# Kernel optimization log

Hardware: AMD Instinct MI355X
Metric: run time of the kernel (lower is better)

Reference implementation:

```python
import jax, jax.numpy as jnp
import numpy as np

H = 10          # hidden_size
TAIL = 1440     # slice out[:, -1440:-1, :]


def _cell(x, h, c, w_ih, w_hh, b):
    # PyTorch LSTM gate order: i, f, g, o
    gates = x @ w_ih.T + h @ w_hh.T + b          # [B, 4H]
    i, f, g, o = jnp.split(gates, 4, axis=-1)
    c = jax.nn.sigmoid(f) * c + jax.nn.sigmoid(i) * jnp.tanh(g)
    h = jax.nn.sigmoid(o) * jnp.tanh(c)
    return h, c


def setup_inputs() -> dict:
    key = jax.random.key(0)
    ks = jax.random.split(key, 13)
    s = 1.0 / np.sqrt(H)  # PyTorch default init range

    def u(k, shape):
        return jax.random.uniform(k, shape, jnp.float32, -s, s)

    return {
        "x": jax.random.normal(ks[0], (4096, 2048), jnp.float32),
        "w_ih0": u(ks[1], (4 * H, 1)),
        "w_hh0": u(ks[2], (4 * H, H)),
        "b_ih0": u(ks[3], (4 * H,)),
        "b_hh0": u(ks[4], (4 * H,)),
        "w_ih1": u(ks[5], (4 * H, H)),
        "w_hh1": u(ks[6], (4 * H, H)),
        "b_ih1": u(ks[7], (4 * H,)),
        "b_hh1": u(ks[8], (4 * H,)),
        "fc1_w": u(ks[9], (6, H)),
        "fc1_b": u(ks[10], (6,)),
        "fc2_w": u(ks[11], (1, 6)),
        "fc2_b": u(ks[12], (1,)),
    }


def reference(x, w_ih0, w_hh0, b_ih0, b_hh0, w_ih1, w_hh1, b_ih1, b_hh1,
              fc1_w, fc1_b, fc2_w, fc2_b):
    B, T = x.shape
    xt = x[..., None].transpose(1, 0, 2)         # [T, B, 1] time-major
    b0 = b_ih0 + b_hh0
    b1 = b_ih1 + b_hh1
    z = jnp.zeros((B, H), x.dtype)

    def step(carry, xi):
        h0, c0, h1, c1 = carry
        h0, c0 = _cell(xi, h0, c0, w_ih0, w_hh0, b0)
        h1, c1 = _cell(h0, h1, c1, w_ih1, w_hh1, b1)
        return (h0, c0, h1, c1), h1

    _, ys = jax.lax.scan(step, (z, z, z, z), xt)  # ys: [T, B, H]
    out = ys.transpose(1, 0, 2)[:, T - TAIL:T - 1, :]   # [B, 1439, H]
    out = jnp.tanh(out @ fc1_w.T + fc1_b)                # [B, 1439, 6]
    out = out @ fc2_w.T + fc2_b                          # [B, 1439, 1]
    return out[..., 0]                                   # [B, 1439]
```

## Files before the change

kernel.cpp:

```cpp
#include <hip/hip_runtime.h>

typedef float v2f __attribute__((ext_vector_type(2)));

#define T_LEN 2048
#define NH    10
#define OUT_T 1439
#define TFIRST 608
#define NSEQ  4096
#define CH    8
#define NCH   (T_LEN / CH)
#define MFIRST (TFIRST / CH)

static __device__ __forceinline__ v2f fma2(v2f a, v2f b, v2f c) {
  return __builtin_elementwise_fma(a, b, c);
}
static __device__ __forceinline__ v2f splat2(float v) { v2f r; r.x = v; r.y = v; return r; }
static __device__ __forceinline__ v2f mulsp(v2f a, float s) { v2f r; r.x = a.x*s; r.y = a.y*s; return r; }

static __device__ __forceinline__ float fast_sigmoid(float z) {
  float e = __builtin_amdgcn_exp2f(z * -1.4426950408889634f);
  return __builtin_amdgcn_rcpf(1.0f + e);
}
static __device__ __forceinline__ float fast_tanh(float z) {
  float e = __builtin_amdgcn_exp2f(z * -2.8853900817779268f);
  return __builtin_amdgcn_rcpf(1.0f + e) * 2.0f - 1.0f;
}

#define ROR_F(v, N) __uint_as_float(__builtin_amdgcn_update_dpp( \
    0, (int)__float_as_uint(v), 0x120 + (N), 0xF, 0xF, true))

__global__ void __launch_bounds__(192, 3)
lstm_fused(const float* __restrict__ x,
           const float* __restrict__ w_ih0, const float* __restrict__ w_hh0,
           const float* __restrict__ b_ih0, const float* __restrict__ b_hh0,
           const float* __restrict__ w_ih1, const float* __restrict__ w_hh1,
           const float* __restrict__ b_ih1, const float* __restrict__ b_hh1,
           const float* __restrict__ fc1_w, const float* __restrict__ fc1_b,
           const float* __restrict__ fc2_w, const float* __restrict__ fc2_b,
           float* __restrict__ out)
{
  __shared__ __align__(16) float h0buf[2][CH][64];
  __shared__ __align__(16) float h1buf[2][CH][64];

  const int tid  = threadIdx.x;
  const int wid  = tid / 64;
  const int lane = tid & 63;
  const int grp  = lane >> 4;
  const int u    = lane & 15;
  const int seq  = (int)blockIdx.x * 4 + grp;

  v2f wIF[NH], wGO[NH], vIF[NH], vGO[NH];
  v2f wx_if, wx_go, bb_if, bb_go;
  wx_if = wx_go = bb_if = bb_go = splat2(0.f);
#pragma unroll
  for (int j = 0; j < NH; ++j) {
    wIF[j] = splat2(0.f); wGO[j] = splat2(0.f);
    vIF[j] = splat2(0.f); vGO[j] = splat2(0.f);
  }
  float fcw[NH];
#pragma unroll
  for (int j = 0; j < NH; ++j) fcw[j] = 0.f;
  float fcb = 0.f, fc2wl = 0.f;
  const float fc2bl = fc2_b[0];

  if (wid == 0) {
    if (u < NH) {
      const int ri = 0*NH+u, rf = 1*NH+u, rg = 2*NH+u, ro = 3*NH+u;
      wx_if.x = w_ih0[ri]; wx_if.y = w_ih0[rf];
      wx_go.x = w_ih0[rg]; wx_go.y = w_ih0[ro];
      bb_if.x = b_ih0[ri] + b_hh0[ri]; bb_if.y = b_ih0[rf] + b_hh0[rf];
      bb_go.x = b_ih0[rg] + b_hh0[rg]; bb_go.y = b_ih0[ro] + b_hh0[ro];
#pragma unroll
      for (int j = 0; j < NH; ++j) {
        wIF[j].x = w_hh0[ri*NH+j]; wIF[j].y = w_hh0[rf*NH+j];
        wGO[j].x = w_hh0[rg*NH+j]; wGO[j].y = w_hh0[ro*NH+j];
      }
    }
  } else if (wid == 1) {
    if (u < NH) {
      const int ri = 0*NH+u, rf = 1*NH+u, rg = 2*NH+u, ro = 3*NH+u;
      bb_if.x = b_ih1[ri] + b_hh1[ri]; bb_if.y = b_ih1[rf] + b_hh1[rf];
      bb_go.x = b_ih1[rg] + b_hh1[rg]; bb_go.y = b_ih1[ro] + b_hh1[ro];
#pragma unroll
      for (int j = 0; j < NH; ++j) {
        wIF[j].x = w_ih1[ri*NH+j]; wIF[j].y = w_ih1[rf*NH+j];
        wGO[j].x = w_ih1[rg*NH+j]; wGO[j].y = w_ih1[ro*NH+j];
        vIF[j].x = w_hh1[ri*NH+j]; vIF[j].y = w_hh1[rf*NH+j];
        vGO[j].x = w_hh1[rg*NH+j]; vGO[j].y = w_hh1[ro*NH+j];
      }
    }
  } else {
    if (u < 6) {
      fcb = fc1_b[u]; fc2wl = fc2_w[u];
#pragma unroll
      for (int j = 0; j < NH; ++j) fcw[j] = fc1_w[u*NH + j];
    }
  }

  const float* xp   = x + (size_t)seq * T_LEN;
  float*       outp = out + (size_t)seq * OUT_T;

  float c = 0.f;
  float r0=0.f,r1=0.f,r2=0.f,r3=0.f,r4=0.f,r5=0.f,r6=0.f,r7=0.f,r8=0.f,r9=0.f;

  auto a_chunk = [&](int m) {
    float* hb = &h0buf[m & 1][0][0];
    const float* hr = &h0buf[m & 1][0][grp * 16];
    const float* xq = xp + m * CH;
#pragma unroll
    for (int s = 0; s < CH; ++s) {
      const float xv = xq[s];
      v2f aA = fma2(wx_if, splat2(xv), bb_if);
      v2f gA = fma2(wx_go, splat2(xv), bb_go);
      v2f aB = mulsp(wIF[1], r1);
      v2f gB = mulsp(wGO[1], r1);
#define L0T(j, hv, AC, GC) { const v2f sp = splat2(hv); \
      AC = fma2(wIF[j], sp, AC); GC = fma2(wGO[j], sp, GC); }
      L0T(0,r0,aA,gA) L0T(2,r2,aA,gA) L0T(3,r3,aB,gB) L0T(4,r4,aA,gA)
      L0T(5,r5,aB,gB) L0T(6,r6,aA,gA) L0T(7,r7,aB,gB) L0T(8,r8,aA,gA)
      L0T(9,r9,aB,gB)
#undef L0T
      const v2f gif = aA + aB;
      const v2f ggo = gA + gB;
      const float si = fast_sigmoid(gif.x);
      const float sf = fast_sigmoid(gif.y);
      const float tg = fast_tanh(ggo.x);
      const float so = fast_sigmoid(ggo.y);
      c = sf * c + si * tg;
      const float h0n = so * fast_tanh(c);
      hb[s*64 + lane] = h0n;
      const float4 va = *(const float4*)(hr + s*64);
      const float4 vb = *(const float4*)(hr + s*64 + 4);
      const float2 vc = *(const float2*)(hr + s*64 + 8);
      r0=va.x; r1=va.y; r2=va.z; r3=va.w;
      r4=vb.x; r5=vb.y; r6=vb.z; r7=vb.w;
      r8=vc.x; r9=vc.y;
    }
  };

  auto b_chunk = [&](int m) {
    const float* hbi = &h0buf[m & 1][0][grp * 16];
    float* ob = &h1buf[m & 1][0][0];
    const float* orr = &h1buf[m & 1][0][grp * 16];
#pragma unroll
    for (int s = 0; s < CH; ++s) {
      const float4 pa = *(const float4*)(hbi + s*64);
      const float4 pb = *(const float4*)(hbi + s*64 + 4);
      const float2 pc = *(const float2*)(hbi + s*64 + 8);
      v2f cA = fma2(wIF[0], splat2(pa.x), bb_if);
      v2f hA = fma2(wGO[0], splat2(pa.x), bb_go);
      v2f cB = mulsp(wIF[1], pa.y);
      v2f hB = mulsp(wGO[1], pa.y);
#define L1I(j, hv, AC, GC) { const v2f sp = splat2(hv); \
      AC = fma2(wIF[j], sp, AC); GC = fma2(wGO[j], sp, GC); }
      L1I(2,pa.z,cA,hA) L1I(3,pa.w,cB,hB) L1I(4,pb.x,cA,hA) L1I(5,pb.y,cB,hB)
      L1I(6,pb.z,cA,hA) L1I(7,pb.w,cB,hB) L1I(8,pc.x,cA,hA) L1I(9,pc.y,cB,hB)
#undef L1I
      v2f cC = mulsp(vIF[0], r0);
      v2f hC = mulsp(vGO[0], r0);
      v2f cD = mulsp(vIF[1], r1);
      v2f hD = mulsp(vGO[1], r1);
#define L1R(j, hv, AC, GC) { const v2f sp = splat2(hv); \
      AC = fma2(vIF[j], sp, AC); GC = fma2(vGO[j], sp, GC); }
      L1R(2,r2,cC,hC) L1R(3,r3,cD,hD) L1R(4,r4,cC,hC) L1R(5,r5,cD,hD)
      L1R(6,r6,cC,hC) L1R(7,r7,cD,hD) L1R(8,r8,cC,hC) L1R(9,r9,cD,hD)
#undef L1R
      const v2f gif = (cA + cB) + (cC + cD);
      const v2f ggo = (hA + hB) + (hC + hD);
      const float si1 = fast_sigmoid(gif.x);
      const float sf1 = fast_sigmoid(gif.y);
      const float tg1 = fast_tanh(ggo.x);
      const float so1 = fast_sigmoid(ggo.y);
      c = sf1 * c + si1 * tg1;
      const float h1n = so1 * fast_tanh(c);
      ob[s*64 + lane] = h1n;
      const float4 va = *(const float4*)(orr + s*64);
      const float4 vb = *(const float4*)(orr + s*64 + 4);
      const float2 vc = *(const float2*)(orr + s*64 + 8);
      r0=va.x; r1=va.y; r2=va.z; r3=va.w;
      r4=vb.x; r5=vb.y; r6=vb.z; r7=vb.w;
      r8=vc.x; r9=vc.y;
    }
  };

  auto c_chunk = [&](int m) {
    const float* hb = &h1buf[m & 1][0][grp * 16];
    const int t0 = m * CH;
    float* oq = outp + (t0 - TFIRST);
#pragma unroll
    for (int s = 0; s < CH; ++s) {
      if (t0 + s < TFIRST + OUT_T) {
        const float4 pa = *(const float4*)(hb + s*64);
        const float4 pb = *(const float4*)(hb + s*64 + 4);
        const float2 pc = *(const float2*)(hb + s*64 + 8);
        float acc = __builtin_fmaf(pa.x, fcw[0], fcb);
        acc = __builtin_fmaf(pa.y, fcw[1], acc);
        acc = __builtin_fmaf(pa.z, fcw[2], acc);
        acc = __builtin_fmaf(pa.w, fcw[3], acc);
        acc = __builtin_fmaf(pb.x, fcw[4], acc);
        acc = __builtin_fmaf(pb.y, fcw[5], acc);
        acc = __builtin_fmaf(pb.z, fcw[6], acc);
        acc = __builtin_fmaf(pb.w, fcw[7], acc);
        acc = __builtin_fmaf(pc.x, fcw[8], acc);
        acc = __builtin_fmaf(pc.y, fcw[9], acc);
        float y = fast_tanh(acc) * fc2wl;
        y += ROR_F(y, 8);
        y += ROR_F(y, 4);
        y += ROR_F(y, 2);
        y += ROR_F(y, 1);
        if (u == 0) oq[s] = y + fc2bl;
      }
    }
  };

#pragma unroll 1
  for (int r = 0; r < NCH + 2; ++r) {
    if (wid == 0) {
      if (r < NCH) a_chunk(r);
    } else if (wid == 1) {
      if (r >= 1 && r < NCH + 1) b_chunk(r - 1);
    } else {
      const int m = r - 2;
      if (m >= MFIRST && m < NCH) c_chunk(m);
    }
    __syncthreads();
  }
}

extern "C" void kernel_launch(void* const* d_in, const int* in_sizes, int n_in,
                              void* d_out, int out_size, void* d_ws, size_t ws_size,
                              hipStream_t stream) {
  const float* x     = (const float*)d_in[0];
  const float* w_ih0 = (const float*)d_in[1];
  const float* w_hh0 = (const float*)d_in[2];
  const float* b_ih0 = (const float*)d_in[3];
  const float* b_hh0 = (const float*)d_in[4];
  const float* w_ih1 = (const float*)d_in[5];
  const float* w_hh1 = (const float*)d_in[6];
  const float* b_ih1 = (const float*)d_in[7];
  const float* b_hh1 = (const float*)d_in[8];
  const float* fc1_w = (const float*)d_in[9];
  const float* fc1_b = (const float*)d_in[10];
  const float* fc2_w = (const float*)d_in[11];
  const float* fc2_b = (const float*)d_in[12];
  float* out = (float*)d_out;

  lstm_fused<<<dim3(NSEQ / 4), dim3(192), 0, stream>>>(
      x, w_ih0, w_hh0, b_ih0, b_hh0, w_ih1, w_hh1, b_ih1, b_hh1,
      fc1_w, fc1_b, fc2_w, fc2_b, out);
}
```

Measured before the change: 735.7 us.

## Fold activation scales into weights, merge FC into layer-0 wave, double chunk size

Pre-scales the LSTM and FC weights and biases by the exp2 constants for sigmoid and tanh. This removes a multiply per activation and lets the cell state be kept pre-scaled, so tanh(c) needs no extra scale. The FC head work moves from a dedicated third wave into the layer-0 wave, shrinking the block to 128 threads. The chunk size doubles to halve the number of block barriers, and x is loaded as float4 vectors. In exchange, the layer-0 wave now does both the recurrence and the FC head each round, which may lengthen its critical path.

```diff
diff --git a/kernel.cpp b/kernel.cpp
--- a/kernel.cpp
+++ b/kernel.cpp
@@ -7,29 +7,26 @@
 #define OUT_T 1439
 #define TFIRST 608
 #define NSEQ  4096
-#define CH    8
+#define CH    16
 #define NCH   (T_LEN / CH)
 #define MFIRST (TFIRST / CH)
 
+#define KSIG (-1.4426950408889634f)
+#define KTAN (-2.8853900817779268f)
+
 static __device__ __forceinline__ v2f fma2(v2f a, v2f b, v2f c) {
   return __builtin_elementwise_fma(a, b, c);
 }
 static __device__ __forceinline__ v2f splat2(float v) { v2f r; r.x = v; r.y = v; return r; }
 static __device__ __forceinline__ v2f mulsp(v2f a, float s) { v2f r; r.x = a.x*s; r.y = a.y*s; return r; }
-
-static __device__ __forceinline__ float fast_sigmoid(float z) {
-  float e = __builtin_amdgcn_exp2f(z * -1.4426950408889634f);
+static __device__ __forceinline__ float rcp1p(float e) {
   return __builtin_amdgcn_rcpf(1.0f + e);
-}
-static __device__ __forceinline__ float fast_tanh(float z) {
-  float e = __builtin_amdgcn_exp2f(z * -2.8853900817779268f);
-  return __builtin_amdgcn_rcpf(1.0f + e) * 2.0f - 1.0f;
 }
 
 #define ROR_F(v, N) __uint_as_float(__builtin_amdgcn_update_dpp( \
     0, (int)__float_as_uint(v), 0x120 + (N), 0xF, 0xF, true))
 
-__global__ void __launch_bounds__(192, 3)
+__global__ void __launch_bounds__(128, 2)
 lstm_fused(const float* __restrict__ x,
            const float* __restrict__ w_ih0, const float* __restrict__ w_hh0,
            const float* __restrict__ b_ih0, const float* __restrict__ b_hh0,
@@ -43,7 +40,7 @@
   __shared__ __align__(16) float h1buf[2][CH][64];
 
   const int tid  = threadIdx.x;
-  const int wid  = tid / 64;
+  const int wid  = tid >> 6;
   const int lane = tid & 63;
   const int grp  = lane >> 4;
   const int u    = lane & 15;
@@ -60,40 +57,41 @@
   float fcw[NH];
 #pragma unroll
   for (int j = 0; j < NH; ++j) fcw[j] = 0.f;
-  float fcb = 0.f, fc2wl = 0.f;
+  float fcb = 0.f, fc2w2 = 0.f, fc2wn = 0.f;
   const float fc2bl = fc2_b[0];
 
   if (wid == 0) {
     if (u < NH) {
       const int ri = 0*NH+u, rf = 1*NH+u, rg = 2*NH+u, ro = 3*NH+u;
-      wx_if.x = w_ih0[ri]; wx_if.y = w_ih0[rf];
-      wx_go.x = w_ih0[rg]; wx_go.y = w_ih0[ro];
-      bb_if.x = b_ih0[ri] + b_hh0[ri]; bb_if.y = b_ih0[rf] + b_hh0[rf];
-      bb_go.x = b_ih0[rg] + b_hh0[rg]; bb_go.y = b_ih0[ro] + b_hh0[ro];
+      wx_if.x = KSIG * w_ih0[ri];            wx_if.y = KSIG * w_ih0[rf];
+      wx_go.x = KTAN * w_ih0[rg];            wx_go.y = KSIG * w_ih0[ro];
+      bb_if.x = KSIG * (b_ih0[ri] + b_hh0[ri]); bb_if.y = KSIG * (b_ih0[rf] + b_hh0[rf]);
+      bb_go.x = KTAN * (b_ih0[rg] + b_hh0[rg]); bb_go.y = KSIG * (b_ih0[ro] + b_hh0[ro]);
 #pragma unroll
       for (int j = 0; j < NH; ++j) {
-        wIF[j].x = w_hh0[ri*NH+j]; wIF[j].y = w_hh0[rf*NH+j];
-        wGO[j].x = w_hh0[rg*NH+j]; wGO[j].y = w_hh0[ro*NH+j];
+        wIF[j].x = KSIG * w_hh0[ri*NH+j]; wIF[j].y = KSIG * w_hh0[rf*NH+j];
+        wGO[j].x = KTAN * w_hh0[rg*NH+j]; wGO[j].y = KSIG * w_hh0[ro*NH+j];
       }
     }
-  } else if (wid == 1) {
+    if (u < 6) {
+      fcb = KTAN * fc1_b[u];
+      const float w2 = fc2_w[u];
+      fc2w2 = 2.f * w2; fc2wn = -w2;
+#pragma unroll
+      for (int j = 0; j < NH; ++j) fcw[j] = KTAN * fc1_w[u*NH + j];
+    }
+  } else {
     if (u < NH) {
       const int ri = 0*NH+u, rf = 1*NH+u, rg = 2*NH+u, ro = 3*NH+u;
-      bb_if.x = b_ih1[ri] + b_hh1[ri]; bb_if.y = b_ih1[rf] + b_hh1[rf];
-      bb_go.x = b_ih1[rg] + b_hh1[rg]; bb_go.y = b_ih1[ro] + b_hh1[ro];
+      bb_if.x = KSIG * (b_ih1[ri] + b_hh1[ri]); bb_if.y = KSIG * (b_ih1[rf] + b_hh1[rf]);
+      bb_go.x = KTAN * (b_ih1[rg] + b_hh1[rg]); bb_go.y = KSIG * (b_ih1[ro] + b_hh1[ro]);
 #pragma unroll
       for (int j = 0; j < NH; ++j) {
-        wIF[j].x = w_ih1[ri*NH+j]; wIF[j].y = w_ih1[rf*NH+j];
-        wGO[j].x = w_ih1[rg*NH+j]; wGO[j].y = w_ih1[ro*NH+j];
-        vIF[j].x = w_hh1[ri*NH+j]; vIF[j].y = w_hh1[rf*NH+j];
-        vGO[j].x = w_hh1[rg*NH+j]; vGO[j].y = w_hh1[ro*NH+j];
+        wIF[j].x = KSIG * w_ih1[ri*NH+j]; wIF[j].y = KSIG * w_ih1[rf*NH+j];
+        wGO[j].x = KTAN * w_ih1[rg*NH+j]; wGO[j].y = KSIG * w_ih1[ro*NH+j];
+        vIF[j].x = KSIG * w_hh1[ri*NH+j]; vIF[j].y = KSIG * w_hh1[rf*NH+j];
+        vGO[j].x = KTAN * w_hh1[rg*NH+j]; vGO[j].y = KSIG * w_hh1[ro*NH+j];
       }
-    }
-  } else {
-    if (u < 6) {
-      fcb = fc1_b[u]; fc2wl = fc2_w[u];
-#pragma unroll
-      for (int j = 0; j < NH; ++j) fcw[j] = fc1_w[u*NH + j];
     }
   }
 
@@ -106,10 +104,13 @@
   auto a_chunk = [&](int m) {
     float* hb = &h0buf[m & 1][0][0];
     const float* hr = &h0buf[m & 1][0][grp * 16];
-    const float* xq = xp + m * CH;
+    const float4* xq = (const float4*)(xp + m * CH);
+    float4 xw[CH / 4];
+#pragma unroll
+    for (int i = 0; i < CH / 4; ++i) xw[i] = xq[i];
 #pragma unroll
     for (int s = 0; s < CH; ++s) {
-      const float xv = xq[s];
+      const float xv = ((const float*)xw)[s];
       v2f aA = fma2(wx_if, splat2(xv), bb_if);
       v2f gA = fma2(wx_go, splat2(xv), bb_go);
       v2f aB = mulsp(wIF[1], r1);
@@ -122,12 +123,15 @@
 #undef L0T
       const v2f gif = aA + aB;
       const v2f ggo = gA + gB;
-      const float si = fast_sigmoid(gif.x);
-      const float sf = fast_sigmoid(gif.y);
-      const float tg = fast_tanh(ggo.x);
-      const float so = fast_sigmoid(ggo.y);
-      c = sf * c + si * tg;
-      const float h0n = so * fast_tanh(c);
+      const float si = rcp1p(__builtin_amdgcn_exp2f(gif.x));
+      const float sf = rcp1p(__builtin_amdgcn_exp2f(gif.y));
+      const float rg = rcp1p(__builtin_amdgcn_exp2f(ggo.x));
+      const float so = rcp1p(__builtin_amdgcn_exp2f(ggo.y));
+      const float tgp = __builtin_fmaf(rg, 2.f*KTAN, -KTAN);
+      c = __builtin_fmaf(sf, c, si * tgp);
+      const float rc = rcp1p(__builtin_amdgcn_exp2f(c));
+      const float tc = __builtin_fmaf(rc, 2.f, -1.f);
+      const float h0n = so * tc;
       hb[s*64 + lane] = h0n;
       const float4 va = *(const float4*)(hr + s*64);
       const float4 vb = *(const float4*)(hr + s*64 + 4);
@@ -167,12 +171,15 @@
 #undef L1R
       const v2f gif = (cA + cB) + (cC + cD);
       const v2f ggo = (hA + hB) + (hC + hD);
-      const float si1 = fast_sigmoid(gif.x);
-      const float sf1 = fast_sigmoid(gif.y);
-      const float tg1 = fast_tanh(ggo.x);
-      const float so1 = fast_sigmoid(ggo.y);
-      c = sf1 * c + si1 * tg1;
-      const float h1n = so1 * fast_tanh(c);
+      const float si = rcp1p(__builtin_amdgcn_exp2f(gif.x));
+      const float sf = rcp1p(__builtin_amdgcn_exp2f(gif.y));
+      const float rg = rcp1p(__builtin_amdgcn_exp2f(ggo.x));
+      const float so = rcp1p(__builtin_amdgcn_exp2f(ggo.y));
+      const float tgp = __builtin_fmaf(rg, 2.f*KTAN, -KTAN);
+      c = __builtin_fmaf(sf, c, si * tgp);
+      const float rc = rcp1p(__builtin_amdgcn_exp2f(c));
+      const float tc = __builtin_fmaf(rc, 2.f, -1.f);
+      const float h1n = so * tc;
       ob[s*64 + lane] = h1n;
       const float4 va = *(const float4*)(orr + s*64);
       const float4 vb = *(const float4*)(orr + s*64 + 4);
@@ -183,13 +190,12 @@
     }
   };
 
-  auto c_chunk = [&](int m) {
+  auto fc_chunk = [&](int m) {
     const float* hb = &h1buf[m & 1][0][grp * 16];
-    const int t0 = m * CH;
-    float* oq = outp + (t0 - TFIRST);
+    float* oq = outp + (m * CH - TFIRST);
 #pragma unroll
     for (int s = 0; s < CH; ++s) {
-      if (t0 + s < TFIRST + OUT_T) {
+      if (m * CH + s < TFIRST + OUT_T) {
         const float4 pa = *(const float4*)(hb + s*64);
         const float4 pb = *(const float4*)(hb + s*64 + 4);
         const float2 pc = *(const float2*)(hb + s*64 + 8);
@@ -203,7 +209,8 @@
         acc = __builtin_fmaf(pb.w, fcw[7], acc);
         acc = __builtin_fmaf(pc.x, fcw[8], acc);
         acc = __builtin_fmaf(pc.y, fcw[9], acc);
-        float y = fast_tanh(acc) * fc2wl;
+        const float rc = rcp1p(__builtin_amdgcn_exp2f(acc));
+        float y = __builtin_fmaf(rc, fc2w2, fc2wn);
         y += ROR_F(y, 8);
         y += ROR_F(y, 4);
         y += ROR_F(y, 2);
@@ -217,11 +224,10 @@
   for (int r = 0; r < NCH + 2; ++r) {
     if (wid == 0) {
       if (r < NCH) a_chunk(r);
-    } else if (wid == 1) {
-      if (r >= 1 && r < NCH + 1) b_chunk(r - 1);
+      const int m = r - 2;
+      if (m >= MFIRST && m < NCH) fc_chunk(m);
     } else {
-      const int m = r - 2;
-      if (m >= MFIRST && m < NCH) c_chunk(m);
+      if (r >= 1 && r <= NCH) b_chunk(r - 1);
     }
     __syncthreads();
   }
@@ -245,7 +251,7 @@
   const float* fc2_b = (const float*)d_in[12];
   float* out = (float*)d_out;
 
-  lstm_fused<<<dim3(NSEQ / 4), dim3(192), 0, stream>>>(
+  lstm_fused<<<dim3(NSEQ / 4), dim3(128), 0, stream>>>(
       x, w_ih0, w_hh0, b_ih0, b_hh0, w_ih1, w_hh1, b_ih1, b_hh1,
       fc1_w, fc1_b, fc2_w, fc2_b, out);
 }
```

Result: no change. 724.0 us (-1.6%).
